# Performance work log

Measured on AMD Instinct MI355X. Metric: run time of the kernel, lower is better.

Reference implementation:

```python
import jax, jax.numpy as jnp
import numpy as np

B, T, C, H = 4, 2048, 1024, 16
D = C // H  # head_dim = 64

def setup_inputs() -> dict:
    key = jax.random.key(0)
    ks = jax.random.split(key, 5)
    scale = 1.0 / np.sqrt(C)
    return {
        "x": jax.random.normal(ks[0], (B, T, C), dtype=jnp.float32),
        "Wq": jax.random.normal(ks[1], (C, C), dtype=jnp.float32) * scale,
        "Wk": jax.random.normal(ks[2], (C, C), dtype=jnp.float32) * scale,
        "Wv": jax.random.normal(ks[3], (C, C), dtype=jnp.float32) * scale,
        "Wo": jax.random.normal(ks[4], (C, C), dtype=jnp.float32) * scale,
        "bo": jnp.zeros((C,), dtype=jnp.float32),
    }

def reference(x, Wq, Wk, Wv, Wo, bo):
    Bx, Tx, Cx = x.shape
    # projections -> [B, H, T, D]
    def split_heads(y):
        return y.reshape(Bx, Tx, H, D).transpose(0, 2, 1, 3)
    Q = split_heads(x @ Wq)
    K = split_heads(x @ Wk)
    V = split_heads(x @ Wv)
    # scaled dot-product with causal mask: [B, H, T, T]
    scores = jnp.einsum('bhqd,bhkd->bhqk', Q, K) / jnp.sqrt(jnp.asarray(D, x.dtype))
    causal = jnp.tril(jnp.ones((Tx, Tx), dtype=bool))
    scores = jnp.where(causal, scores, -jnp.inf)
    weights = jax.nn.softmax(scores, axis=-1)
    attn = jnp.einsum('bhqk,bhkd->bhqd', weights, V)  # [B, H, T, D]
    out = attn.transpose(0, 2, 1, 3).reshape(Bx, Tx, Cx)
    return out @ Wo + bo
```

## Files before the change

### kernel.cpp

```cpp
#include <hip/hip_runtime.h>
#include <hip/hip_bf16.h>
#include <cmath>

typedef __bf16 bf16;
typedef __bf16 bf16x8 __attribute__((ext_vector_type(8)));
typedef __bf16 bf16x4v __attribute__((ext_vector_type(4)));
typedef float f32x4 __attribute__((ext_vector_type(4)));

#define B_ 4
#define T_ 2048
#define C_ 1024
#define H_ 16
#define D_ 64
#define BT_ 8192
#define LOG2E 1.4426950408889634f

__device__ __forceinline__ void async_cp16(const void* g, void* l) {
  __builtin_amdgcn_global_load_lds(
      (__attribute__((address_space(1))) void*)g,
      (__attribute__((address_space(3))) void*)l, 16, 0, 0);
}

__device__ __forceinline__ f32x4 mfma16(bf16x8 a, bf16x8 b, f32x4 c) {
  return __builtin_amdgcn_mfma_f32_16x16x32_bf16(a, b, c, 0, 0, 0);
}

__global__ __launch_bounds__(256) void prep_kernel(
    const float* __restrict__ x, const float* __restrict__ Wq,
    const float* __restrict__ Wk, const float* __restrict__ Wv,
    const float* __restrict__ Wo, bf16* __restrict__ xb,
    bf16* __restrict__ wt) {
  __shared__ float tile[32][33];
  const int id = blockIdx.x;
  const int t = threadIdx.x;
  if (id < 8192) {
    const int i = id * 256 + t;
    float4 v = ((const float4*)x)[i];
    bf16x4v o = {(bf16)v.x, (bf16)v.y, (bf16)v.z, (bf16)v.w};
    ((bf16x4v*)xb)[i] = o;
    return;
  }
  const int id2 = id - 8192;
  const int z = id2 >> 10;
  const float* W = (z == 0) ? Wq : (z == 1) ? Wk : (z == 2) ? Wv : Wo;
  bf16* Wt = wt + (size_t)z * 1048576;
  const int bx = id2 & 31, by = (id2 >> 5) & 31;
  const int xx = t & 31, yy = t >> 5;
  const int n0 = bx * 32, k0 = by * 32;
#pragma unroll
  for (int j = 0; j < 32; j += 8)
    tile[yy + j][xx] = W[(size_t)(k0 + yy + j) * C_ + n0 + xx];
  __syncthreads();
#pragma unroll
  for (int j = 0; j < 32; j += 8)
    Wt[(size_t)(n0 + yy + j) * C_ + k0 + xx] = (bf16)tile[xx][yy + j];
}

template <int F32OUT>
__device__ __forceinline__ void gemm_tile_db(
    const bf16* __restrict__ A, const bf16* __restrict__ Bt,
    void* __restrict__ Cv, const float* __restrict__ bias, int M, int N, int K,
    int m0, int n0, bf16* As, bf16* Bs) {
  const int t = threadIdx.x;
  const int lane = t & 63;
  const int wave = t >> 6;
  const int quad = lane >> 4;
  const int l15 = lane & 15;
  const int wm = (wave >> 1) * 64;
  const int wn = (wave & 1) * 64;

  const int srow = t >> 2;
  const int sc0 = (t & 3) ^ (srow & 3);
  const bf16* Ag = A + (size_t)(m0 + srow) * K + sc0 * 8;
  const bf16* Ag2 = A + (size_t)(m0 + 64 + srow) * K + sc0 * 8;
  const bf16* Bg = Bt + (size_t)(n0 + srow) * K + sc0 * 8;
  const bf16* Bg2 = Bt + (size_t)(n0 + 64 + srow) * K + sc0 * 8;

  const int niter = K >> 5;
  auto stage = [&](int kt, int buf) {
    bf16* Ad = As + buf * 4096 + t * 8;
    bf16* Bd = Bs + buf * 4096 + t * 8;
    async_cp16(Ag + kt * 32, Ad);
    async_cp16(Ag2 + kt * 32, Ad + 2048);
    async_cp16(Bg + kt * 32, Bd);
    async_cp16(Bg2 + kt * 32, Bd + 2048);
  };

  f32x4 acc[4][4] = {};
  stage(0, 0);

  for (int kt = 0; kt < niter; kt++) {
    __syncthreads();
    if (kt + 1 < niter) stage(kt + 1, (kt + 1) & 1);
    const bf16* Ab = As + (kt & 1) * 4096;
    const bf16* Bb = Bs + (kt & 1) * 4096;
    bf16x8 af[4], bfr[4];
#pragma unroll
    for (int i = 0; i < 4; i++) {
      const int r = wm + i * 16 + l15;
      af[i] = *(const bf16x8*)&Ab[r * 32 + ((quad ^ (r & 3)) * 8)];
    }
#pragma unroll
    for (int j = 0; j < 4; j++) {
      const int r = wn + j * 16 + l15;
      bfr[j] = *(const bf16x8*)&Bb[r * 32 + ((quad ^ (r & 3)) * 8)];
    }
#pragma unroll
    for (int i = 0; i < 4; i++)
#pragma unroll
      for (int j = 0; j < 4; j++)
        acc[i][j] = mfma16(af[i], bfr[j], acc[i][j]);
  }

#pragma unroll
  for (int i = 0; i < 4; i++) {
    const int gr = m0 + wm + i * 16 + quad * 4;
#pragma unroll
    for (int j = 0; j < 4; j++) {
      const int gc = n0 + wn + j * 16 + l15;
      const float bv = F32OUT ? bias[gc] : 0.0f;
#pragma unroll
      for (int r = 0; r < 4; r++) {
        const float v = acc[i][j][r] + bv;
        if (F32OUT)
          ((float*)Cv)[(size_t)(gr + r) * N + gc] = v;
        else
          ((bf16*)Cv)[(size_t)(gr + r) * N + gc] = (bf16)v;
      }
    }
  }
}

__global__ __launch_bounds__(256, 4) void qkv_gemm_kernel(
    const bf16* __restrict__ xb, const bf16* __restrict__ wqkvT,
    bf16* __restrict__ qkb, bf16* __restrict__ vtb) {
  __shared__ __align__(16) bf16 As[2 * 4096];
  __shared__ __align__(16) bf16 Bs[2 * 4096];
  int id = blockIdx.x;
  if (id < 1024) {
    gemm_tile_db<0>(xb, wqkvT, (void*)qkb, nullptr, 8192, 2048, 1024,
                    (id >> 4) * 128, (id & 15) * 128, As, Bs);
  } else {
    id -= 1024;
    gemm_tile_db<0>(wqkvT + 2 * 1024 * 1024, xb, (void*)vtb, nullptr, 1024,
                    8192, 1024, (id >> 6) * 128, (id & 63) * 128, As, Bs);
  }
}

__global__ __launch_bounds__(256, 4) void out_gemm_kernel(
    const bf16* __restrict__ attn, const bf16* __restrict__ woT,
    float* __restrict__ out, const float* __restrict__ bo) {
  __shared__ __align__(16) bf16 As[2 * 4096];
  __shared__ __align__(16) bf16 Bs[2 * 4096];
  const int id = blockIdx.x;
  gemm_tile_db<1>(attn, woT, (void*)out, bo, 8192, 1024, 1024,
                  (id >> 3) * 128, (id & 7) * 128, As, Bs);
}

__global__ __launch_bounds__(256, 3) void flash_attn_kernel(
    const bf16* __restrict__ qk, const bf16* __restrict__ vt,
    bf16* __restrict__ attn) {
  __shared__ __align__(16) char smem[51200];
  bf16* KsB = (bf16*)smem;
  bf16* VsB = (bf16*)(smem + 16384);
  bf16* Ps = (bf16*)(smem + 32768);

  const int t = threadIdx.x;
  const int lane = t & 63;
  const int wave = t >> 6;
  const int quad = lane >> 4;
  const int l15 = lane & 15;
  const int l7 = l15 & 7;
  const int bx = blockIdx.x;
  const int qt = 15 - (bx >> 6);
  const int bh = bx & 63;
  const int b = bh >> 4;
  const int h = bh & 15;

  const bf16* Qg = qk + (size_t)b * T_ * 2048 + h * 64;
  const bf16* Kg = qk + (size_t)b * T_ * 2048 + 1024 + h * 64;
  const bf16* Vg = vt + (size_t)h * 64 * BT_ + b * T_;

  const float QSCALE = 0.125f * LOG2E;
  bf16x8 qf[2][2];
  const int qrow0 = qt * 128 + wave * 32;
#pragma unroll
  for (int mt = 0; mt < 2; mt++)
#pragma unroll
    for (int ks = 0; ks < 2; ks++) {
      bf16x8 v = *(const bf16x8*)(Qg + (size_t)(qrow0 + mt * 16 + l15) * 2048 +
                                  ks * 32 + quad * 8);
#pragma unroll
      for (int j = 0; j < 8; j++) v[j] = (bf16)((float)v[j] * QSCALE);
      qf[mt][ks] = v;
    }

  f32x4 o_acc[4][2] = {};
  f32x4 l4[2] = {};

  const int sr8 = lane >> 3;
  const int sc = (lane & 7) ^ sr8;

  auto stage = [&](int j64, int buf) {
    const int k0 = j64 * 64;
    bf16* KL = KsB + buf * 4096 + wave * 1024 + lane * 8;
    const bf16* KG = Kg + (size_t)(k0 + wave * 16 + sr8) * 2048 + sc * 8;
    async_cp16(KG, KL);
    async_cp16(KG + (size_t)8 * 2048, KL + 512);
    bf16* VL = VsB + buf * 4096 + wave * 1024 + lane * 8;
    const bf16* VG = Vg + (size_t)(wave * 16 + sr8) * BT_ + k0 + sc * 8;
    async_cp16(VG, VL);
    async_cp16(VG + (size_t)8 * BT_, VL + 512);
  };

  const int S = 2 * qt + 2;
  stage(0, 0);

  for (int s = 0; s < S; s++) {
    __syncthreads();
    if (s + 1 < S) stage(s + 1, (s + 1) & 1);
    const bf16* Kb = KsB + (s & 1) * 4096;
    const bf16* Vb = VsB + (s & 1) * 4096;
    const int k0 = s * 64;
    const bool diag = (s >= 2 * qt);

    bf16x4v p[2][4];
#pragma unroll
    for (int kt = 0; kt < 4; kt++) {
      const bf16x8 kf0 =
          *(const bf16x8*)&Kb[(kt * 16 + l15) * 64 + ((quad ^ l7) * 8)];
      const bf16x8 kf1 =
          *(const bf16x8*)&Kb[(kt * 16 + l15) * 64 + (((4 + quad) ^ l7) * 8)];
#pragma unroll
      for (int mt = 0; mt < 2; mt++) {
        f32x4 sv = mfma16(kf0, qf[mt][0], f32x4{0.f, 0.f, 0.f, 0.f});
        sv = mfma16(kf1, qf[mt][1], sv);
        if (diag) {
          const int qg = qt * 128 + wave * 32 + mt * 16 + l15;
#pragma unroll
          for (int i = 0; i < 4; i++)
            if (k0 + kt * 16 + quad * 4 + i > qg) sv[i] = -INFINITY;
        }
        f32x4 e;
#pragma unroll
        for (int i = 0; i < 4; i++) e[i] = __builtin_amdgcn_exp2f(sv[i]);
        l4[mt] += e;
        p[mt][kt] = bf16x4v{(bf16)e[0], (bf16)e[1], (bf16)e[2], (bf16)e[3]};
      }
    }

#pragma unroll
    for (int mt = 0; mt < 2; mt++) {
      const int row = wave * 32 + mt * 16 + l15;
#pragma unroll
      for (int kt = 0; kt < 4; kt++)
        *(bf16x4v*)&Ps[row * 72 + kt * 16 + quad * 4] = p[mt][kt];
    }

#pragma unroll
    for (int ks2 = 0; ks2 < 2; ks2++) {
      bf16x8 pa[2], vb[4];
#pragma unroll
      for (int mt = 0; mt < 2; mt++)
        pa[mt] = *(const bf16x8*)&Ps[(wave * 32 + mt * 16 + l15) * 72 +
                                     ks2 * 32 + quad * 8];
#pragma unroll
      for (int dt = 0; dt < 4; dt++)
        vb[dt] = *(const bf16x8*)&Vb[(dt * 16 + l15) * 64 +
                                     (((ks2 * 4 + quad) ^ l7) * 8)];
#pragma unroll
      for (int dt = 0; dt < 4; dt++)
#pragma unroll
        for (int mt = 0; mt < 2; mt++)
          o_acc[dt][mt] = mfma16(vb[dt], pa[mt], o_acc[dt][mt]);
    }
  }

  float inv[2];
#pragma unroll
  for (int mt = 0; mt < 2; mt++) {
    float l = l4[mt][0] + l4[mt][1] + l4[mt][2] + l4[mt][3];
    l += __shfl_xor(l, 16, 64);
    l += __shfl_xor(l, 32, 64);
    inv[mt] = 1.0f / l;
  }
#pragma unroll
  for (int dt = 0; dt < 4; dt++)
#pragma unroll
    for (int mt = 0; mt < 2; mt++) {
      const int q = qt * 128 + wave * 32 + mt * 16 + l15;
      bf16x4v o = {(bf16)(o_acc[dt][mt][0] * inv[mt]),
                   (bf16)(o_acc[dt][mt][1] * inv[mt]),
                   (bf16)(o_acc[dt][mt][2] * inv[mt]),
                   (bf16)(o_acc[dt][mt][3] * inv[mt])};
      *(bf16x4v*)(attn + (size_t)(b * T_ + q) * 1024 + h * 64 + dt * 16 +
                  quad * 4) = o;
    }
}

extern "C" void kernel_launch(void* const* d_in, const int* in_sizes, int n_in,
                              void* d_out, int out_size, void* d_ws,
                              size_t ws_size, hipStream_t stream) {
  const float* x = (const float*)d_in[0];
  const float* Wq = (const float*)d_in[1];
  const float* Wk = (const float*)d_in[2];
  const float* Wv = (const float*)d_in[3];
  const float* Wo = (const float*)d_in[4];
  const float* bo = (const float*)d_in[5];
  float* out = (float*)d_out;

  char* ws = (char*)d_ws;
  bf16* xb = (bf16*)(ws);
  bf16* qkb = (bf16*)(ws + 16777216);
  bf16* vtb = (bf16*)(ws + 50331648);
  bf16* attn = (bf16*)(ws + 67108864);
  bf16* wqkvT = (bf16*)(ws + 83886080);

  prep_kernel<<<12288, 256, 0, stream>>>(x, Wq, Wk, Wv, Wo, xb, wqkvT);

  qkv_gemm_kernel<<<1536, 256, 0, stream>>>(xb, wqkvT, qkb, vtb);

  flash_attn_kernel<<<1024, 256, 0, stream>>>(qkb, vtb, attn);

  out_gemm_kernel<<<512, 256, 0, stream>>>(attn, wqkvT + 3 * 1024 * 1024, out,
                                           bo);
}
```

Before: 239.8 us.

## Use 8-way XOR LDS swizzle and XCD-aware tile mapping in GEMMs

```diff
diff --git a/kernel.cpp b/kernel.cpp
--- a/kernel.cpp
+++ b/kernel.cpp
@@ -69,12 +69,14 @@
   const int wm = (wave >> 1) * 64;
   const int wn = (wave & 1) * 64;
 
-  const int srow = t >> 2;
-  const int sc0 = (t & 3) ^ (srow & 3);
-  const bf16* Ag = A + (size_t)(m0 + srow) * K + sc0 * 8;
-  const bf16* Ag2 = A + (size_t)(m0 + 64 + srow) * K + sc0 * 8;
-  const bf16* Bg = Bt + (size_t)(n0 + srow) * K + sc0 * 8;
-  const bf16* Bg2 = Bt + (size_t)(n0 + 64 + srow) * K + sc0 * 8;
+  const int u = (t & 7) ^ ((t >> 3) & 7);
+  const int sh = u >> 2;
+  const int scx = u & 3;
+  const int r0 = (t >> 3) + 64 * sh;
+  const bf16* Ag = A + (size_t)(m0 + r0) * K + scx * 8;
+  const bf16* Ag2 = A + (size_t)(m0 + r0 + 32) * K + scx * 8;
+  const bf16* Bg = Bt + (size_t)(n0 + r0) * K + scx * 8;
+  const bf16* Bg2 = Bt + (size_t)(n0 + r0 + 32) * K + scx * 8;
 
   const int niter = K >> 5;
   auto stage = [&](int kt, int buf) {
@@ -98,12 +100,16 @@
 #pragma unroll
     for (int i = 0; i < 4; i++) {
       const int r = wm + i * 16 + l15;
-      af[i] = *(const bf16x8*)&Ab[r * 32 + ((quad ^ (r & 3)) * 8)];
+      const int L = r & 63;
+      af[i] = *(const bf16x8*)
+          &Ab[L * 64 + ((((r >> 6) * 4 + quad) ^ (L & 7)) * 8)];
     }
 #pragma unroll
     for (int j = 0; j < 4; j++) {
       const int r = wn + j * 16 + l15;
-      bfr[j] = *(const bf16x8*)&Bb[r * 32 + ((quad ^ (r & 3)) * 8)];
+      const int L = r & 63;
+      bfr[j] = *(const bf16x8*)
+          &Bb[L * 64 + ((((r >> 6) * 4 + quad) ^ (L & 7)) * 8)];
     }
 #pragma unroll
     for (int i = 0; i < 4; i++)
@@ -138,12 +144,18 @@
   __shared__ __align__(16) bf16 Bs[2 * 4096];
   int id = blockIdx.x;
   if (id < 1024) {
-    gemm_tile_db<0>(xb, wqkvT, (void*)qkb, nullptr, 8192, 2048, 1024,
-                    (id >> 4) * 128, (id & 15) * 128, As, Bs);
+    const int xcd = id & 7, rest = id >> 3;
+    const int mt = rest >> 1;
+    const int nt = xcd * 2 + (rest & 1);
+    gemm_tile_db<0>(xb, wqkvT, (void*)qkb, nullptr, 8192, 2048, 1024, mt * 128,
+                    nt * 128, As, Bs);
   } else {
     id -= 1024;
+    const int xcd = id & 7, rest = id >> 3;
+    const int mt = rest >> 3;
+    const int nt = xcd * 8 + (rest & 7);
     gemm_tile_db<0>(wqkvT + 2 * 1024 * 1024, xb, (void*)vtb, nullptr, 1024,
-                    8192, 1024, (id >> 6) * 128, (id & 63) * 128, As, Bs);
+                    8192, 1024, mt * 128, nt * 128, As, Bs);
   }
 }
 
@@ -153,8 +165,11 @@
   __shared__ __align__(16) bf16 As[2 * 4096];
   __shared__ __align__(16) bf16 Bs[2 * 4096];
   const int id = blockIdx.x;
-  gemm_tile_db<1>(attn, woT, (void*)out, bo, 8192, 1024, 1024,
-                  (id >> 3) * 128, (id & 7) * 128, As, Bs);
+  const int xcd = id & 7, rest = id >> 3;
+  const int nt = rest & 7;
+  const int mt = xcd + (rest >> 3) * 8;
+  gemm_tile_db<1>(attn, woT, (void*)out, bo, 8192, 1024, 1024, mt * 128,
+                  nt * 128, As, Bs);
 }
 
 __global__ __launch_bounds__(256, 3) void flash_attn_kernel(
```

Result: faster. 235.0 us (-2.0%).
